# Kernel optimization log

Measured on AMD Instinct MI355X. Metric: run time of the kernel, lower is better.

The kernel has to match this reference:

```python
import jax, jax.numpy as jnp
import numpy as np

N, M, D, G, E = 1024, 1024, 1024, 16, 64  # rois, ref rois, feat_dim, groups, emb_dim
DG = D // G  # 64 per-group dim


def _make_boxes(k, n):
    k1, k2 = jax.random.split(k)
    xy = jax.random.uniform(k1, (n, 2), dtype=jnp.float32) * 500.0
    wh = jax.random.uniform(k2, (n, 2), dtype=jnp.float32) * 100.0 + 1.0
    return jnp.concatenate([xy, xy + wh], axis=1)  # [n,4] xmin,ymin,xmax,ymax


def setup_inputs() -> dict:
    key = jax.random.key(0)
    ks = jax.random.split(key, 10)
    s = 0.02
    return {
        "roi_feat": jax.random.normal(ks[0], (N, D), dtype=jnp.float32),
        "ref_feat": jax.random.normal(ks[1], (M, D), dtype=jnp.float32),
        "rois1": _make_boxes(ks[2], N),
        "rois2": _make_boxes(ks[3], M),
        "Wq": jax.random.normal(ks[4], (D, D), dtype=jnp.float32) * s,
        "bq": jnp.zeros((D,), jnp.float32),
        "Wk": jax.random.normal(ks[5], (D, D), dtype=jnp.float32) * s,
        "bk": jnp.zeros((D,), jnp.float32),
        "Wg": jax.random.normal(ks[6], (G, E), dtype=jnp.float32) * s,
        "bg": jnp.zeros((G,), jnp.float32),
        "Wv": jax.random.normal(ks[7], (G, DG, D), dtype=jnp.float32) * s,
        "bv": jnp.zeros((D,), jnp.float32),
    }


def _position_matrix(bbox, ref_bbox):
    # bbox [N,4], ref_bbox [M,4] -> [N,M,4]
    def parts(b):
        xmin, ymin, xmax, ymax = b[:, 0], b[:, 1], b[:, 2], b[:, 3]
        w = xmax - xmin + 1.0
        h = ymax - ymin + 1.0
        cx = 0.5 * (xmin + xmax)
        cy = 0.5 * (ymin + ymax)
        return w, h, cx, cy

    w, h, cx, cy = parts(bbox)            # [N]
    wr, hr, cxr, cyr = parts(ref_bbox)    # [M]
    dx = jnp.log(jnp.abs((cx[:, None] - cxr[None, :]) / w[:, None]) + 1e-3)
    dy = jnp.log(jnp.abs((cy[:, None] - cyr[None, :]) / h[:, None]) + 1e-3)
    dw = jnp.log(w[:, None] / wr[None, :])
    dh = jnp.log(h[:, None] / hr[None, :])
    return jnp.stack([dx, dy, dw, dh], axis=2)  # [N,M,4]


def _position_embedding(pos_mat, feat_dim=64, wave_length=1000.0):
    fr = jnp.arange(feat_dim // 8, dtype=jnp.float32)            # [8]
    dim_mat = jnp.power(wave_length, (8.0 / feat_dim) * fr)      # [8]
    div = pos_mat[..., None] * 100.0 / dim_mat                   # [N,M,4,8]
    emb = jnp.concatenate([jnp.sin(div), jnp.cos(div)], axis=3)  # [N,M,4,16]
    return emb.reshape(pos_mat.shape[0], pos_mat.shape[1], -1)   # [N,M,64]


def reference(roi_feat, ref_feat, rois1, rois2, Wq, bq, Wk, bk, Wg, bg, Wv, bv):
    # position embedding: [N,M,E]
    pos_emb = _position_embedding(_position_matrix(rois1, rois2), feat_dim=E)
    # Wgs 1x1 conv (E -> G) + relu -> aff_weight [N,G,M]
    aff_weight = jax.nn.relu(jnp.einsum("nme,ge->ngm", pos_emb, Wg) + bg[None, :, None])
    # grouped q/k projections
    q = (roi_feat @ Wq + bq).reshape(N, G, DG)   # [N,G,dg]
    k = (ref_feat @ Wk + bk).reshape(M, G, DG)   # [M,G,dg]
    aff = jnp.einsum("ngd,mgd->ngm", q, k) * (1.0 / np.sqrt(DG))
    weighted = jnp.log(aff_weight + 1e-6) + aff  # [N,G,M]
    sm = jax.nn.softmax(weighted, axis=2)
    out_t = jnp.einsum("ngm,md->ngd", sm, ref_feat)          # [N,G,D]
    out = jnp.einsum("ngd,god->ngo", out_t, Wv).reshape(N, D) + bv  # grouped 1x1 conv
    return out
```

## Files before the change

kernel.cpp:

```cpp
#include <hip/hip_runtime.h>
#include <hip/hip_fp16.h>
#include <cstddef>

#define N_ 1024
#define M_ 1024
#define D_ 1024
#define G_ 16
#define DG_ 64

typedef __bf16 bf16x8 __attribute__((ext_vector_type(8)));
typedef _Float16 f16x8 __attribute__((ext_vector_type(8)));
typedef float f32x4 __attribute__((ext_vector_type(4)));

__device__ __forceinline__ size_t qkf_idx(int g, int rb, int ks, int lane) {
    return ((((size_t)(g * 64 + rb)) * 2 + ks) * 64 + lane) * 8;
}
__device__ __forceinline__ size_t vf_idx(int g, int ot, int mc, int lane) {
    return ((((size_t)(g * 4 + ot)) * 32 + mc) * 64 + lane) * 8;
}
__device__ __forceinline__ size_t awt_idx(int g, int mb, int n, int quad) {
    return (((size_t)(g * 64 + mb)) * 1024 + n) * 16 + quad * 4;
}

__global__ __launch_bounds__(256)
void transpose_cast(const float* __restrict__ Wq, const float* __restrict__ Wk,
                    __bf16* __restrict__ WqT, __bf16* __restrict__ WkT)
{
    __shared__ float t[64][65];
    const float* src = blockIdx.z ? Wk : Wq;
    __bf16* dst = blockIdx.z ? WkT : WqT;
    const int i0 = blockIdx.x * 64, j0 = blockIdx.y * 64;
    const int tid = threadIdx.x;
    const int r = tid >> 4, c4 = (tid & 15) * 4;
    #pragma unroll
    for (int it = 0; it < 4; ++it) {
        float4 a = *(const float4*)&src[(size_t)(i0 + r + it * 16) * D_ + j0 + c4];
        t[r + it * 16][c4 + 0] = a.x; t[r + it * 16][c4 + 1] = a.y;
        t[r + it * 16][c4 + 2] = a.z; t[r + it * 16][c4 + 3] = a.w;
    }
    __syncthreads();
    #pragma unroll
    for (int it = 0; it < 4; ++it) {
        const int row = r + it * 16;
        __bf16 p[4];
        #pragma unroll
        for (int q = 0; q < 4; ++q) p[q] = (__bf16)t[c4 + q][row];
        *(uint2*)&dst[(size_t)(j0 + row) * D_ + i0 + c4] = *(const uint2*)p;
    }
}

__global__ __launch_bounds__(256)
void cast_wv(const float* __restrict__ Wv, __bf16* __restrict__ out)
{
    const int idx = blockIdx.x * 256 + threadIdx.x;
    float4 a = *(const float4*)&Wv[(size_t)idx * 4];
    __bf16 p[4] = {(__bf16)a.x, (__bf16)a.y, (__bf16)a.z, (__bf16)a.w};
    *(uint2*)&out[(size_t)idx * 4] = *(const uint2*)p;
}

__global__ __launch_bounds__(256)
void gemm_mfma(const float* __restrict__ roi, const float* __restrict__ ref,
               const __bf16* __restrict__ WqT, const __bf16* __restrict__ WkT,
               const __bf16* __restrict__ Wvb,
               const float* __restrict__ bq, const float* __restrict__ bk,
               __bf16* __restrict__ Qf, __bf16* __restrict__ Kf,
               __bf16* __restrict__ Vf)
{
    __shared__ __bf16 As[128][72];
    __shared__ __bf16 Bs[128][72];
    const int z = blockIdx.z;
    const float* A = (z == 0) ? roi : ref;
    const __bf16* B = (z == 0) ? WqT : (z == 1) ? WkT : Wvb;
    const int tid = threadIdx.x;
    const int i0 = blockIdx.x * 128, j0 = blockIdx.y * 128;
    const int w = tid >> 6, lane = tid & 63;
    const int quad = lane >> 4, l15 = lane & 15;
    const int iw = (w & 1) * 64, jw = (w >> 1) * 64;

    f32x4 acc[4][4] = {};

    for (int k0 = 0; k0 < D_; k0 += 64) {
        __syncthreads();
        #pragma unroll
        for (int it = 0; it < 8; ++it) {
            const int idx = tid + 256 * it;
            const int row = idx >> 4, c = idx & 15;
            float4 a = *(const float4*)&A[(size_t)(i0 + row) * D_ + k0 + c * 4];
            __bf16* d = &As[row][c * 4];
            d[0] = (__bf16)a.x; d[1] = (__bf16)a.y; d[2] = (__bf16)a.z; d[3] = (__bf16)a.w;
        }
        #pragma unroll
        for (int it = 0; it < 4; ++it) {
            const int idx = tid + 256 * it;
            const int row = idx >> 3, c = idx & 7;
            *(uint4*)&Bs[row][c * 8] = *(const uint4*)&B[(size_t)(j0 + row) * D_ + k0 + c * 8];
        }
        __syncthreads();
        #pragma unroll
        for (int ks = 0; ks < 2; ++ks) {
            bf16x8 af[4], bfr[4];
            #pragma unroll
            for (int t = 0; t < 4; ++t) {
                af[t]  = *(const bf16x8*)&As[iw + t * 16 + l15][ks * 32 + quad * 8];
                bfr[t] = *(const bf16x8*)&Bs[jw + t * 16 + l15][ks * 32 + quad * 8];
            }
            #pragma unroll
            for (int ti = 0; ti < 4; ++ti)
                #pragma unroll
                for (int tj = 0; tj < 4; ++tj)
                    acc[ti][tj] = __builtin_amdgcn_mfma_f32_16x16x32_bf16(
                        af[ti], bfr[tj], acc[ti][tj], 0, 0, 0);
        }
    }

    if (z < 2) {
        const float* bias = (z == 0) ? bq : bk;
        __bf16* dst = (z == 0) ? Qf : Kf;
        const float scale = (z == 0) ? 0.125f : 1.0f;
        #pragma unroll
        for (int ti = 0; ti < 4; ++ti) {
            const int rbase = i0 + iw + ti * 16;
            const int rb = rbase >> 4;
            #pragma unroll
            for (int tj = 0; tj < 4; ++tj) {
                const int go = j0 + jw + tj * 16 + l15;
                const int g = go >> 6, ks = (go >> 5) & 1;
                const int lanef = ((go >> 3) & 3) * 16;
                const int jf = go & 7;
                const float bb = bias[go];
                __bf16* base = dst + qkf_idx(g, rb, ks, 0) + jf;
                #pragma unroll
                for (int r = 0; r < 4; ++r)
                    base[(size_t)(lanef + quad * 4 + r) * 8] =
                        (__bf16)((acc[ti][tj][r] + bb) * scale);
            }
        }
    } else {
        #pragma unroll
        for (int ti = 0; ti < 4; ++ti) {
            const int mbase = i0 + iw + ti * 16 + quad * 4;
            const int mc = mbase >> 5, quadv = (mbase >> 3) & 3, jb = mbase & 7;
            #pragma unroll
            for (int tj = 0; tj < 4; ++tj) {
                const int go = j0 + jw + tj * 16 + l15;
                const int g = go >> 6, ot = (go >> 4) & 3, o15 = go & 15;
                __bf16 p[4];
                #pragma unroll
                for (int r = 0; r < 4; ++r) p[r] = (__bf16)acc[ti][tj][r];
                *(uint2*)&Vf[vf_idx(g, ot, mc, quadv * 16 + o15) + jb] = *(const uint2*)p;
            }
        }
    }
}

__global__ __launch_bounds__(256)
void posbias_mfma(const float* __restrict__ rois1, const float* __restrict__ rois2,
                  const float* __restrict__ Wg, const float* __restrict__ bg,
                  __half* __restrict__ AWt)
{
    const int tid = threadIdx.x;
    const int w = tid >> 6, lane = tid & 63;
    const int quad = lane >> 4, l15 = lane & 15;
    const int n = blockIdx.y;
    const int m0w = blockIdx.x * 256 + w * 64;

    const float xmin = rois1[n * 4 + 0], ymin = rois1[n * 4 + 1];
    const float xmax = rois1[n * 4 + 2], ymax = rois1[n * 4 + 3];
    const float wn  = xmax - xmin + 1.f, hn  = ymax - ymin + 1.f;
    const float cxn = 0.5f * (xmin + xmax), cyn = 0.5f * (ymin + ymax);

    f16x8 wgf[2];
    #pragma unroll
    for (int ks = 0; ks < 2; ++ks) {
        const float* p = &Wg[l15 * 64 + ks * 32 + quad * 8];
        float4 a = *(const float4*)p;
        float4 b = *(const float4*)(p + 4);
        wgf[ks][0] = (_Float16)a.x; wgf[ks][1] = (_Float16)a.y;
        wgf[ks][2] = (_Float16)a.z; wgf[ks][3] = (_Float16)a.w;
        wgf[ks][4] = (_Float16)b.x; wgf[ks][5] = (_Float16)b.y;
        wgf[ks][6] = (_Float16)b.z; wgf[ks][7] = (_Float16)b.w;
    }
    const float bgv = bg[l15];

    const float fr8[8] = {100.0f, 42.16965f, 17.782794f, 7.4989421f,
                          3.1622777f, 1.3335214f, 0.56234133f, 0.23713737f};
    const float phase = (quad & 1) ? 1.5707963267948966f : 0.f;

    #pragma unroll
    for (int ti = 0; ti < 4; ++ti) {
        const int mt0 = m0w + ti * 16;
        const int m = mt0 + l15;
        float4 r2 = *(const float4*)&rois2[m * 4];
        const float wr  = r2.z - r2.x + 1.f, hr  = r2.w - r2.y + 1.f;
        const float cxr = 0.5f * (r2.x + r2.z), cyr = 0.5f * (r2.y + r2.w);

        const float f0 = __logf(fabsf((cxn - cxr) / wn) + 0.001f);
        const float f1 = __logf(fabsf((cyn - cyr) / hn) + 0.001f);
        const float f2 = __logf(wn / wr);
        const float f3 = __logf(hn / hr);
        const float fa = (quad & 2) ? f1 : f0;
        const float fb = (quad & 2) ? f3 : f2;

        f32x4 acc = {};
        #pragma unroll
        for (int ks = 0; ks < 2; ++ks) {
            const float feat = ks ? fb : fa;
            f16x8 ef;
            #pragma unroll
            for (int j = 0; j < 8; ++j)
                ef[j] = (_Float16)__sinf(fmaf(feat, fr8[j], phase));
            acc = __builtin_amdgcn_mfma_f32_16x16x32_f16(ef, wgf[ks], acc, 0, 0, 0);
        }

        __half p[4];
        #pragma unroll
        for (int r = 0; r < 4; ++r)
            p[r] = __float2half(fmaxf(acc[r] + bgv, 0.f) + 1e-6f);
        *(uint2*)&AWt[awt_idx(l15, mt0 >> 4, n, quad)] = *(const uint2*)p;
    }
}

__global__ __launch_bounds__(256)
void attn_mfma(const __bf16* __restrict__ Qf, const __bf16* __restrict__ Kf,
               const __bf16* __restrict__ Vf, const __half* __restrict__ AWt,
               const float* __restrict__ bv, float* __restrict__ out)
{
    __shared__ __bf16 Ps[4][2][16][72];
    __shared__ float accb[4][64][17];
    __shared__ float lsb[4][16];

    const int tid = threadIdx.x;
    const int w = tid >> 6, lane = tid & 63;
    const int quad = lane >> 4, l15 = lane & 15;
    const int nb = blockIdx.x, n0 = nb * 16, g = blockIdx.y;

    bf16x8 qf[2];
    qf[0] = *(const bf16x8*)&Qf[qkf_idx(g, nb, 0, lane)];
    qf[1] = *(const bf16x8*)&Qf[qkf_idx(g, nb, 1, lane)];

    f32x4 acc[4] = {};
    float llocal = 0.f;

    #pragma unroll
    for (int t64 = 0; t64 < 4; ++t64) {
        const int mt = w * 4 + t64;
        const int buf = t64 & 1;

        f32x4 s[4];
        #pragma unroll
        for (int t = 0; t < 4; ++t) {
            bf16x8 ka0 = *(const bf16x8*)&Kf[qkf_idx(g, mt * 4 + t, 0, lane)];
            bf16x8 ka1 = *(const bf16x8*)&Kf[qkf_idx(g, mt * 4 + t, 1, lane)];
            f32x4 z = {};
            z = __builtin_amdgcn_mfma_f32_16x16x32_bf16(ka0, qf[0], z, 0, 0, 0);
            s[t] = __builtin_amdgcn_mfma_f32_16x16x32_bf16(ka1, qf[1], z, 0, 0, 0);
        }

        #pragma unroll
        for (int t = 0; t < 4; ++t) {
            uint2 au = *(const uint2*)&AWt[awt_idx(g, mt * 4 + t, n0 + l15, quad)];
            const __half* a4 = (const __half*)&au;
            __bf16 pk[4];
            #pragma unroll
            for (int r = 0; r < 4; ++r) {
                const float p = __half2float(a4[r]) * __expf(s[t][r]);
                llocal += p;
                pk[r] = (__bf16)p;
            }
            *(uint2*)&Ps[w][buf][l15][t * 16 + quad * 4] = *(const uint2*)pk;
        }

        #pragma unroll
        for (int mcl = 0; mcl < 2; ++mcl) {
            bf16x8 pb = *(const bf16x8*)&Ps[w][buf][l15][mcl * 32 + quad * 8];
            #pragma unroll
            for (int ot = 0; ot < 4; ++ot) {
                bf16x8 va = *(const bf16x8*)&Vf[vf_idx(g, ot, mt * 2 + mcl, lane)];
                acc[ot] = __builtin_amdgcn_mfma_f32_16x16x32_bf16(va, pb, acc[ot], 0, 0, 0);
            }
        }
    }

    llocal += __shfl_xor(llocal, 16, 64);
    llocal += __shfl_xor(llocal, 32, 64);

    #pragma unroll
    for (int ot = 0; ot < 4; ++ot)
        #pragma unroll
        for (int r = 0; r < 4; ++r)
            accb[w][ot * 16 + quad * 4 + r][l15] = acc[ot][r];
    if (quad == 0) lsb[w][l15] = llocal;
    __syncthreads();

    const float lt = lsb[0][l15] + lsb[1][l15] + lsb[2][l15] + lsb[3][l15];
    const float inv = 1.f / lt;
    #pragma unroll
    for (int r = 0; r < 4; ++r) {
        const int o = w * 16 + quad * 4 + r;
        const int ogl = g * 64 + o;
        const float v = accb[0][o][l15] + accb[1][o][l15] +
                        accb[2][o][l15] + accb[3][o][l15];
        out[(size_t)(n0 + l15) * D_ + ogl] = v * inv + bv[ogl];
    }
}

extern "C" void kernel_launch(void* const* d_in, const int* in_sizes, int n_in,
                              void* d_out, int out_size, void* d_ws, size_t ws_size,
                              hipStream_t stream) {
    const float* roi_feat = (const float*)d_in[0];
    const float* ref_feat = (const float*)d_in[1];
    const float* rois1    = (const float*)d_in[2];
    const float* rois2    = (const float*)d_in[3];
    const float* Wq       = (const float*)d_in[4];
    const float* bq       = (const float*)d_in[5];
    const float* Wk       = (const float*)d_in[6];
    const float* bk       = (const float*)d_in[7];
    const float* Wg       = (const float*)d_in[8];
    const float* bg       = (const float*)d_in[9];
    const float* Wv       = (const float*)d_in[10];
    const float* bv       = (const float*)d_in[11];
    float* out = (float*)d_out;

    char* ws = (char*)d_ws;
    __bf16* WqT = (__bf16*)(ws + 0);
    __bf16* WkT = (__bf16*)(ws + (2u << 20));
    __bf16* Wvb = (__bf16*)(ws + (4u << 20));
    __bf16* Qf  = (__bf16*)(ws + (6u << 20));
    __bf16* Kf  = (__bf16*)(ws + (8u << 20));
    __bf16* Vf  = (__bf16*)(ws + (10u << 20));
    __half* AWt = (__half*)(ws + (12u << 20));

    dim3 blk(256);
    transpose_cast<<<dim3(16, 16, 2), blk, 0, stream>>>(Wq, Wk, WqT, WkT);
    cast_wv<<<dim3(1024), blk, 0, stream>>>(Wv, Wvb);
    posbias_mfma<<<dim3(4, 1024), blk, 0, stream>>>(rois1, rois2, Wg, bg, AWt);
    gemm_mfma<<<dim3(8, 8, 3), blk, 0, stream>>>(roi_feat, ref_feat, WqT, WkT, Wvb,
                                                 bq, bk, Qf, Kf, Vf);
    attn_mfma<<<dim3(64, 16), blk, 0, stream>>>(Qf, Kf, Vf, AWt, bv, out);
}
```

Before: 163.0 us.

## Double-buffer GEMM tiles, stage outputs through LDS, use row-major intermediates

```diff
diff --git a/kernel.cpp b/kernel.cpp
--- a/kernel.cpp
+++ b/kernel.cpp
@@ -12,26 +12,31 @@
 typedef _Float16 f16x8 __attribute__((ext_vector_type(8)));
 typedef float f32x4 __attribute__((ext_vector_type(4)));
 
-__device__ __forceinline__ size_t qkf_idx(int g, int rb, int ks, int lane) {
-    return ((((size_t)(g * 64 + rb)) * 2 + ks) * 64 + lane) * 8;
-}
-__device__ __forceinline__ size_t vf_idx(int g, int ot, int mc, int lane) {
-    return ((((size_t)(g * 4 + ot)) * 32 + mc) * 64 + lane) * 8;
-}
-__device__ __forceinline__ size_t awt_idx(int g, int mb, int n, int quad) {
-    return (((size_t)(g * 64 + mb)) * 1024 + n) * 16 + quad * 4;
-}
-
 __global__ __launch_bounds__(256)
-void transpose_cast(const float* __restrict__ Wq, const float* __restrict__ Wk,
-                    __bf16* __restrict__ WqT, __bf16* __restrict__ WkT)
+void prep_weights(const float* __restrict__ Wq, const float* __restrict__ Wk,
+                  const float* __restrict__ Wv,
+                  __bf16* __restrict__ WqT, __bf16* __restrict__ WkT,
+                  __bf16* __restrict__ Wvb)
 {
-    __shared__ float t[64][65];
-    const float* src = blockIdx.z ? Wk : Wq;
-    __bf16* dst = blockIdx.z ? WkT : WqT;
+    const int z = blockIdx.z;
     const int i0 = blockIdx.x * 64, j0 = blockIdx.y * 64;
     const int tid = threadIdx.x;
     const int r = tid >> 4, c4 = (tid & 15) * 4;
+
+    if (z == 2) {
+        #pragma unroll
+        for (int it = 0; it < 4; ++it) {
+            const int row = r + it * 16;
+            float4 a = *(const float4*)&Wv[(size_t)(i0 + row) * D_ + j0 + c4];
+            __bf16 p[4] = {(__bf16)a.x, (__bf16)a.y, (__bf16)a.z, (__bf16)a.w};
+            *(uint2*)&Wvb[(size_t)(i0 + row) * D_ + j0 + c4] = *(const uint2*)p;
+        }
+        return;
+    }
+
+    __shared__ float t[64][65];
+    const float* src = z ? Wk : Wq;
+    __bf16* dst = z ? WkT : WqT;
     #pragma unroll
     for (int it = 0; it < 4; ++it) {
         float4 a = *(const float4*)&src[(size_t)(i0 + r + it * 16) * D_ + j0 + c4];
@@ -49,25 +54,19 @@
     }
 }
 
-__global__ __launch_bounds__(256)
-void cast_wv(const float* __restrict__ Wv, __bf16* __restrict__ out)
-{
-    const int idx = blockIdx.x * 256 + threadIdx.x;
-    float4 a = *(const float4*)&Wv[(size_t)idx * 4];
-    __bf16 p[4] = {(__bf16)a.x, (__bf16)a.y, (__bf16)a.z, (__bf16)a.w};
-    *(uint2*)&out[(size_t)idx * 4] = *(const uint2*)p;
-}
-
-__global__ __launch_bounds__(256)
+#define GP 72
+#define CTP 136
+
+__global__ __launch_bounds__(256, 1)
 void gemm_mfma(const float* __restrict__ roi, const float* __restrict__ ref,
                const __bf16* __restrict__ WqT, const __bf16* __restrict__ WkT,
                const __bf16* __restrict__ Wvb,
                const float* __restrict__ bq, const float* __restrict__ bk,
-               __bf16* __restrict__ Qf, __bf16* __restrict__ Kf,
-               __bf16* __restrict__ Vf)
+               __bf16* __restrict__ qout, __bf16* __restrict__ kout,
+               __bf16* __restrict__ Vt)
 {
-    __shared__ __bf16 As[128][72];
-    __shared__ __bf16 Bs[128][72];
+    __shared__ __align__(16) char smem[2 * 2 * 128 * GP * 2];
+
     const int z = blockIdx.z;
     const float* A = (z == 0) ? roi : ref;
     const __bf16* B = (z == 0) ? WqT : (z == 1) ? WkT : Wvb;
@@ -77,32 +76,56 @@
     const int quad = lane >> 4, l15 = lane & 15;
     const int iw = (w & 1) * 64, jw = (w >> 1) * 64;
 
+    const int arow = tid >> 4, ac = (tid & 15) * 4;
+    const int brow = tid >> 3, bc = (tid & 7) * 8;
+
     f32x4 acc[4][4] = {};
-
-    for (int k0 = 0; k0 < D_; k0 += 64) {
-        __syncthreads();
+    float4 ra[8];
+    uint4 rb[4];
+
+    auto As = [&](int buf) { return (__bf16(*)[GP])(smem + buf * 36864); };
+    auto Bs = [&](int buf) { return (__bf16(*)[GP])(smem + buf * 36864 + 18432); };
+
+    auto load_tile = [&](int kt) {
+        const int k0 = kt * 64;
+        #pragma unroll
+        for (int it = 0; it < 8; ++it)
+            ra[it] = *(const float4*)&A[(size_t)(i0 + arow + it * 16) * D_ + k0 + ac];
+        #pragma unroll
+        for (int it = 0; it < 4; ++it)
+            rb[it] = *(const uint4*)&B[(size_t)(j0 + brow + it * 32) * D_ + k0 + bc];
+    };
+    auto write_tile = [&](int buf) {
+        __bf16(*as)[GP] = As(buf);
+        __bf16(*bs)[GP] = Bs(buf);
         #pragma unroll
         for (int it = 0; it < 8; ++it) {
-            const int idx = tid + 256 * it;
-            const int row = idx >> 4, c = idx & 15;
-            float4 a = *(const float4*)&A[(size_t)(i0 + row) * D_ + k0 + c * 4];
-            __bf16* d = &As[row][c * 4];
-            d[0] = (__bf16)a.x; d[1] = (__bf16)a.y; d[2] = (__bf16)a.z; d[3] = (__bf16)a.w;
-        }
-        #pragma unroll
-        for (int it = 0; it < 4; ++it) {
-            const int idx = tid + 256 * it;
-            const int row = idx >> 3, c = idx & 7;
-            *(uint4*)&Bs[row][c * 8] = *(const uint4*)&B[(size_t)(j0 + row) * D_ + k0 + c * 8];
-        }
-        __syncthreads();
+            __bf16 p[4] = {(__bf16)ra[it].x, (__bf16)ra[it].y,
+                           (__bf16)ra[it].z, (__bf16)ra[it].w};
+            *(uint2*)&as[arow + it * 16][ac] = *(const uint2*)p;
+        }
+        #pragma unroll
+        for (int it = 0; it < 4; ++it)
+            *(uint4*)&bs[brow + it * 32][bc] = rb[it];
+    };
+
+    load_tile(0);
+    write_tile(0);
+    __syncthreads();
+
+    for (int kt = 0; kt < 16; ++kt) {
+        const int buf = kt & 1;
+        if (kt < 15) load_tile(kt + 1);
+
+        __bf16(*as)[GP] = As(buf);
+        __bf16(*bs)[GP] = Bs(buf);
         #pragma unroll
         for (int ks = 0; ks < 2; ++ks) {
             bf16x8 af[4], bfr[4];
             #pragma unroll
             for (int t = 0; t < 4; ++t) {
-                af[t]  = *(const bf16x8*)&As[iw + t * 16 + l15][ks * 32 + quad * 8];
-                bfr[t] = *(const bf16x8*)&Bs[jw + t * 16 + l15][ks * 32 + quad * 8];
+                af[t]  = *(const bf16x8*)&as[iw + t * 16 + l15][ks * 32 + quad * 8];
+                bfr[t] = *(const bf16x8*)&bs[jw + t * 16 + l15][ks * 32 + quad * 8];
             }
             #pragma unroll
             for (int ti = 0; ti < 4; ++ti)
@@ -111,53 +134,58 @@
                     acc[ti][tj] = __builtin_amdgcn_mfma_f32_16x16x32_bf16(
                         af[ti], bfr[tj], acc[ti][tj], 0, 0, 0);
         }
-    }
+
+        if (kt < 15) write_tile(buf ^ 1);
+        __syncthreads();
+    }
+
+    __bf16(*Ct)[CTP] = (__bf16(*)[CTP])smem;
 
     if (z < 2) {
         const float* bias = (z == 0) ? bq : bk;
-        __bf16* dst = (z == 0) ? Qf : Kf;
         const float scale = (z == 0) ? 0.125f : 1.0f;
         #pragma unroll
-        for (int ti = 0; ti < 4; ++ti) {
-            const int rbase = i0 + iw + ti * 16;
-            const int rb = rbase >> 4;
+        for (int ti = 0; ti < 4; ++ti)
             #pragma unroll
             for (int tj = 0; tj < 4; ++tj) {
-                const int go = j0 + jw + tj * 16 + l15;
-                const int g = go >> 6, ks = (go >> 5) & 1;
-                const int lanef = ((go >> 3) & 3) * 16;
-                const int jf = go & 7;
-                const float bb = bias[go];
-                __bf16* base = dst + qkf_idx(g, rb, ks, 0) + jf;
+                const int col = jw + tj * 16 + l15;
+                const float bb = bias[j0 + col];
                 #pragma unroll
                 for (int r = 0; r < 4; ++r)
-                    base[(size_t)(lanef + quad * 4 + r) * 8] =
+                    Ct[iw + ti * 16 + quad * 4 + r][col] =
                         (__bf16)((acc[ti][tj][r] + bb) * scale);
             }
-        }
     } else {
         #pragma unroll
-        for (int ti = 0; ti < 4; ++ti) {
-            const int mbase = i0 + iw + ti * 16 + quad * 4;
-            const int mc = mbase >> 5, quadv = (mbase >> 3) & 3, jb = mbase & 7;
+        for (int ti = 0; ti < 4; ++ti)
             #pragma unroll
             for (int tj = 0; tj < 4; ++tj) {
-                const int go = j0 + jw + tj * 16 + l15;
-                const int g = go >> 6, ot = (go >> 4) & 3, o15 = go & 15;
+                const int col = jw + tj * 16 + l15;
+                const int row0 = iw + ti * 16 + quad * 4;
                 __bf16 p[4];
                 #pragma unroll
                 for (int r = 0; r < 4; ++r) p[r] = (__bf16)acc[ti][tj][r];
-                *(uint2*)&Vf[vf_idx(g, ot, mc, quadv * 16 + o15) + jb] = *(const uint2*)p;
-            }
-        }
-    }
+                *(uint2*)&Ct[col][row0] = *(const uint2*)p;
+            }
+    }
+    __syncthreads();
+
+    __bf16* dst = (z == 0) ? qout : (z == 1) ? kout : Vt;
+    const int orow = tid >> 1, ohalf = (tid & 1) * 64;
+    __bf16* gp = dst + (size_t)((z < 2 ? i0 : j0) + orow) * 1024 +
+                 (z < 2 ? j0 : i0) + ohalf;
+    #pragma unroll
+    for (int c = 0; c < 8; ++c)
+        *(uint4*)&gp[c * 8] = *(const uint4*)&Ct[orow][ohalf + c * 8];
 }
 
 __global__ __launch_bounds__(256)
 void posbias_mfma(const float* __restrict__ rois1, const float* __restrict__ rois2,
                   const float* __restrict__ Wg, const float* __restrict__ bg,
-                  __half* __restrict__ AWt)
+                  __half* __restrict__ aw)
 {
+    __shared__ __half pt[4][16][72];
+
     const int tid = threadIdx.x;
     const int w = tid >> 6, lane = tid & 63;
     const int quad = lane >> 4, l15 = lane & 15;
@@ -216,13 +244,18 @@
         #pragma unroll
         for (int r = 0; r < 4; ++r)
             p[r] = __float2half(fmaxf(acc[r] + bgv, 0.f) + 1e-6f);
-        *(uint2*)&AWt[awt_idx(l15, mt0 >> 4, n, quad)] = *(const uint2*)p;
-    }
+        *(uint2*)&pt[w][l15][ti * 16 + quad * 4] = *(const uint2*)p;
+    }
+
+    const int gg = lane >> 2, mseg = (lane & 3) * 16;
+    __half* dst = aw + (size_t)gg * N_ * M_ + (size_t)n * M_ + m0w + mseg;
+    *(uint4*)&dst[0] = *(const uint4*)&pt[w][gg][mseg];
+    *(uint4*)&dst[8] = *(const uint4*)&pt[w][gg][mseg + 8];
 }
 
 __global__ __launch_bounds__(256)
-void attn_mfma(const __bf16* __restrict__ Qf, const __bf16* __restrict__ Kf,
-               const __bf16* __restrict__ Vf, const __half* __restrict__ AWt,
+void attn_mfma(const __bf16* __restrict__ qb, const __bf16* __restrict__ kb,
+               const __bf16* __restrict__ Vt, const __half* __restrict__ aw,
                const float* __restrict__ bv, float* __restrict__ out)
 {
     __shared__ __bf16 Ps[4][2][16][72];
@@ -235,8 +268,8 @@
     const int nb = blockIdx.x, n0 = nb * 16, g = blockIdx.y;
 
     bf16x8 qf[2];
-    qf[0] = *(const bf16x8*)&Qf[qkf_idx(g, nb, 0, lane)];
-    qf[1] = *(const bf16x8*)&Qf[qkf_idx(g, nb, 1, lane)];
+    qf[0] = *(const bf16x8*)&qb[(size_t)(n0 + l15) * D_ + g * 64 + quad * 8];
+    qf[1] = *(const bf16x8*)&qb[(size_t)(n0 + l15) * D_ + g * 64 + 32 + quad * 8];
 
     f32x4 acc[4] = {};
     float llocal = 0.f;
@@ -244,21 +277,24 @@
     #pragma unroll
     for (int t64 = 0; t64 < 4; ++t64) {
         const int mt = w * 4 + t64;
+        const int m0 = mt * 64;
         const int buf = t64 & 1;
 
         f32x4 s[4];
         #pragma unroll
         for (int t = 0; t < 4; ++t) {
-            bf16x8 ka0 = *(const bf16x8*)&Kf[qkf_idx(g, mt * 4 + t, 0, lane)];
-            bf16x8 ka1 = *(const bf16x8*)&Kf[qkf_idx(g, mt * 4 + t, 1, lane)];
-            f32x4 z = {};
-            z = __builtin_amdgcn_mfma_f32_16x16x32_bf16(ka0, qf[0], z, 0, 0, 0);
-            s[t] = __builtin_amdgcn_mfma_f32_16x16x32_bf16(ka1, qf[1], z, 0, 0, 0);
+            const __bf16* kr = &kb[(size_t)(m0 + t * 16 + l15) * D_ + g * 64 + quad * 8];
+            bf16x8 ka0 = *(const bf16x8*)kr;
+            bf16x8 ka1 = *(const bf16x8*)(kr + 32);
+            f32x4 zz = {};
+            zz = __builtin_amdgcn_mfma_f32_16x16x32_bf16(ka0, qf[0], zz, 0, 0, 0);
+            s[t] = __builtin_amdgcn_mfma_f32_16x16x32_bf16(ka1, qf[1], zz, 0, 0, 0);
         }
 
         #pragma unroll
         for (int t = 0; t < 4; ++t) {
-            uint2 au = *(const uint2*)&AWt[awt_idx(g, mt * 4 + t, n0 + l15, quad)];
+            uint2 au = *(const uint2*)&aw[((size_t)g * N_ + n0 + l15) * M_ +
+                                          m0 + t * 16 + quad * 4];
             const __half* a4 = (const __half*)&au;
             __bf16 pk[4];
             #pragma unroll
@@ -275,7 +311,8 @@
             bf16x8 pb = *(const bf16x8*)&Ps[w][buf][l15][mcl * 32 + quad * 8];
             #pragma unroll
             for (int ot = 0; ot < 4; ++ot) {
-                bf16x8 va = *(const bf16x8*)&Vf[vf_idx(g, ot, mt * 2 + mcl, lane)];
+                bf16x8 va = *(const bf16x8*)&Vt[(size_t)(g * 64 + ot * 16 + l15) * M_ +
+                                                m0 + mcl * 32 + quad * 8];
                 acc[ot] = __builtin_amdgcn_mfma_f32_16x16x32_bf16(va, pb, acc[ot], 0, 0, 0);
             }
         }
@@ -322,19 +359,18 @@
     float* out = (float*)d_out;
 
     char* ws = (char*)d_ws;
-    __bf16* WqT = (__bf16*)(ws + 0);
-    __bf16* WkT = (__bf16*)(ws + (2u << 20));
-    __bf16* Wvb = (__bf16*)(ws + (4u << 20));
-    __bf16* Qf  = (__bf16*)(ws + (6u << 20));
-    __bf16* Kf  = (__bf16*)(ws + (8u << 20));
-    __bf16* Vf  = (__bf16*)(ws + (10u << 20));
-    __half* AWt = (__half*)(ws + (12u << 20));
+    __bf16* WqT  = (__bf16*)(ws + 0);
+    __bf16* WkT  = (__bf16*)(ws + (2u << 20));
+    __bf16* Wvb  = (__bf16*)(ws + (4u << 20));
+    __bf16* qbuf = (__bf16*)(ws + (6u << 20));
+    __bf16* kbuf = (__bf16*)(ws + (8u << 20));
+    __bf16* Vtb  = (__bf16*)(ws + (10u << 20));
+    __half* aw   = (__half*)(ws + (12u << 20));
 
     dim3 blk(256);
-    transpose_cast<<<dim3(16, 16, 2), blk, 0, stream>>>(Wq, Wk, WqT, WkT);
-    cast_wv<<<dim3(1024), blk, 0, stream>>>(Wv, Wvb);
-    posbias_mfma<<<dim3(4, 1024), blk, 0, stream>>>(rois1, rois2, Wg, bg, AWt);
+    prep_weights<<<dim3(16, 16, 3), blk, 0, stream>>>(Wq, Wk, Wv, WqT, WkT, Wvb);
+    posbias_mfma<<<dim3(4, 1024), blk, 0, stream>>>(rois1, rois2, Wg, bg, aw);
     gemm_mfma<<<dim3(8, 8, 3), blk, 0, stream>>>(roi_feat, ref_feat, WqT, WkT, Wvb,
-                                                 bq, bk, Qf, Kf, Vf);
-    attn_mfma<<<dim3(64, 16), blk, 0, stream>>>(Qf, Kf, Vf, AWt, bv, out);
-}
+                                                 bq, bk, qbuf, kbuf, Vtb);
+    attn_mfma<<<dim3(64, 16), blk, 0, stream>>>(qbuf, kbuf, Vtb, aw, bv, out);
+}
```

Measured after the change: 191.2 us. 1.17x slower.

## Merge weight-prep kernels and run GEMM and posbias in one launch

Applied to the files above, without the earlier changes.

```diff
diff --git a/kernel.cpp b/kernel.cpp
--- a/kernel.cpp
+++ b/kernel.cpp
@@ -23,15 +23,30 @@
 }
 
 __global__ __launch_bounds__(256)
-void transpose_cast(const float* __restrict__ Wq, const float* __restrict__ Wk,
-                    __bf16* __restrict__ WqT, __bf16* __restrict__ WkT)
+void prep_weights(const float* __restrict__ Wq, const float* __restrict__ Wk,
+                  const float* __restrict__ Wv,
+                  __bf16* __restrict__ WqT, __bf16* __restrict__ WkT,
+                  __bf16* __restrict__ Wvb)
 {
-    __shared__ float t[64][65];
-    const float* src = blockIdx.z ? Wk : Wq;
-    __bf16* dst = blockIdx.z ? WkT : WqT;
+    const int z = blockIdx.z;
     const int i0 = blockIdx.x * 64, j0 = blockIdx.y * 64;
     const int tid = threadIdx.x;
     const int r = tid >> 4, c4 = (tid & 15) * 4;
+
+    if (z == 2) {
+        #pragma unroll
+        for (int it = 0; it < 4; ++it) {
+            const int row = r + it * 16;
+            float4 a = *(const float4*)&Wv[(size_t)(i0 + row) * D_ + j0 + c4];
+            __bf16 p[4] = {(__bf16)a.x, (__bf16)a.y, (__bf16)a.z, (__bf16)a.w};
+            *(uint2*)&Wvb[(size_t)(i0 + row) * D_ + j0 + c4] = *(const uint2*)p;
+        }
+        return;
+    }
+
+    __shared__ float t[64][65];
+    const float* src = z ? Wk : Wq;
+    __bf16* dst = z ? WkT : WqT;
     #pragma unroll
     for (int it = 0; it < 4; ++it) {
         float4 a = *(const float4*)&src[(size_t)(i0 + r + it * 16) * D_ + j0 + c4];
@@ -50,119 +65,114 @@
 }
 
 __global__ __launch_bounds__(256)
-void cast_wv(const float* __restrict__ Wv, __bf16* __restrict__ out)
-{
-    const int idx = blockIdx.x * 256 + threadIdx.x;
-    float4 a = *(const float4*)&Wv[(size_t)idx * 4];
-    __bf16 p[4] = {(__bf16)a.x, (__bf16)a.y, (__bf16)a.z, (__bf16)a.w};
-    *(uint2*)&out[(size_t)idx * 4] = *(const uint2*)p;
-}
-
-__global__ __launch_bounds__(256)
-void gemm_mfma(const float* __restrict__ roi, const float* __restrict__ ref,
+void fused_mid(const float* __restrict__ roi, const float* __restrict__ ref,
                const __bf16* __restrict__ WqT, const __bf16* __restrict__ WkT,
                const __bf16* __restrict__ Wvb,
                const float* __restrict__ bq, const float* __restrict__ bk,
                __bf16* __restrict__ Qf, __bf16* __restrict__ Kf,
-               __bf16* __restrict__ Vf)
+               __bf16* __restrict__ Vf,
+               const float* __restrict__ rois1, const float* __restrict__ rois2,
+               const float* __restrict__ Wg, const float* __restrict__ bg,
+               __half* __restrict__ AWt)
 {
-    __shared__ __bf16 As[128][72];
-    __shared__ __bf16 Bs[128][72];
-    const int z = blockIdx.z;
-    const float* A = (z == 0) ? roi : ref;
-    const __bf16* B = (z == 0) ? WqT : (z == 1) ? WkT : Wvb;
-    const int tid = threadIdx.x;
-    const int i0 = blockIdx.x * 128, j0 = blockIdx.y * 128;
-    const int w = tid >> 6, lane = tid & 63;
-    const int quad = lane >> 4, l15 = lane & 15;
-    const int iw = (w & 1) * 64, jw = (w >> 1) * 64;
-
-    f32x4 acc[4][4] = {};
-
-    for (int k0 = 0; k0 < D_; k0 += 64) {
-        __syncthreads();
-        #pragma unroll
-        for (int it = 0; it < 8; ++it) {
-            const int idx = tid + 256 * it;
-            const int row = idx >> 4, c = idx & 15;
-            float4 a = *(const float4*)&A[(size_t)(i0 + row) * D_ + k0 + c * 4];
-            __bf16* d = &As[row][c * 4];
-            d[0] = (__bf16)a.x; d[1] = (__bf16)a.y; d[2] = (__bf16)a.z; d[3] = (__bf16)a.w;
-        }
-        #pragma unroll
-        for (int it = 0; it < 4; ++it) {
-            const int idx = tid + 256 * it;
-            const int row = idx >> 3, c = idx & 7;
-            *(uint4*)&Bs[row][c * 8] = *(const uint4*)&B[(size_t)(j0 + row) * D_ + k0 + c * 8];
-        }
-        __syncthreads();
-        #pragma unroll
-        for (int ks = 0; ks < 2; ++ks) {
-            bf16x8 af[4], bfr[4];
-            #pragma unroll
-            for (int t = 0; t < 4; ++t) {
-                af[t]  = *(const bf16x8*)&As[iw + t * 16 + l15][ks * 32 + quad * 8];
-                bfr[t] = *(const bf16x8*)&Bs[jw + t * 16 + l15][ks * 32 + quad * 8];
-            }
-            #pragma unroll
-            for (int ti = 0; ti < 4; ++ti)
-                #pragma unroll
-                for (int tj = 0; tj < 4; ++tj)
-                    acc[ti][tj] = __builtin_amdgcn_mfma_f32_16x16x32_bf16(
-                        af[ti], bfr[tj], acc[ti][tj], 0, 0, 0);
-        }
-    }
-
-    if (z < 2) {
-        const float* bias = (z == 0) ? bq : bk;
-        __bf16* dst = (z == 0) ? Qf : Kf;
-        const float scale = (z == 0) ? 0.125f : 1.0f;
-        #pragma unroll
-        for (int ti = 0; ti < 4; ++ti) {
-            const int rbase = i0 + iw + ti * 16;
-            const int rb = rbase >> 4;
-            #pragma unroll
-            for (int tj = 0; tj < 4; ++tj) {
-                const int go = j0 + jw + tj * 16 + l15;
-                const int g = go >> 6, ks = (go >> 5) & 1;
-                const int lanef = ((go >> 3) & 3) * 16;
-                const int jf = go & 7;
-                const float bb = bias[go];
-                __bf16* base = dst + qkf_idx(g, rb, ks, 0) + jf;
-                #pragma unroll
-                for (int r = 0; r < 4; ++r)
-                    base[(size_t)(lanef + quad * 4 + r) * 8] =
-                        (__bf16)((acc[ti][tj][r] + bb) * scale);
-            }
-        }
-    } else {
-        #pragma unroll
-        for (int ti = 0; ti < 4; ++ti) {
-            const int mbase = i0 + iw + ti * 16 + quad * 4;
-            const int mc = mbase >> 5, quadv = (mbase >> 3) & 3, jb = mbase & 7;
-            #pragma unroll
-            for (int tj = 0; tj < 4; ++tj) {
-                const int go = j0 + jw + tj * 16 + l15;
-                const int g = go >> 6, ot = (go >> 4) & 3, o15 = go & 15;
-                __bf16 p[4];
-                #pragma unroll
-                for (int r = 0; r < 4; ++r) p[r] = (__bf16)acc[ti][tj][r];
-                *(uint2*)&Vf[vf_idx(g, ot, mc, quadv * 16 + o15) + jb] = *(const uint2*)p;
-            }
-        }
-    }
-}
-
-__global__ __launch_bounds__(256)
-void posbias_mfma(const float* __restrict__ rois1, const float* __restrict__ rois2,
-                  const float* __restrict__ Wg, const float* __restrict__ bg,
-                  __half* __restrict__ AWt)
-{
+    __shared__ __align__(16) char smem[36864];
+    const int b = blockIdx.x;
     const int tid = threadIdx.x;
     const int w = tid >> 6, lane = tid & 63;
     const int quad = lane >> 4, l15 = lane & 15;
-    const int n = blockIdx.y;
-    const int m0w = blockIdx.x * 256 + w * 64;
+
+    if (b < 192) {
+        const int z = b >> 6, t6 = b & 63;
+        const float* A = (z == 0) ? roi : ref;
+        const __bf16* B = (z == 0) ? WqT : (z == 1) ? WkT : Wvb;
+        const int i0 = (t6 >> 3) * 128, j0 = (t6 & 7) * 128;
+        const int iw = (w & 1) * 64, jw = (w >> 1) * 64;
+
+        __bf16(*As)[72] = (__bf16(*)[72])smem;
+        __bf16(*Bs)[72] = (__bf16(*)[72])(smem + 18432);
+
+        f32x4 acc[4][4] = {};
+
+        for (int k0 = 0; k0 < D_; k0 += 64) {
+            __syncthreads();
+            #pragma unroll
+            for (int it = 0; it < 8; ++it) {
+                const int idx = tid + 256 * it;
+                const int row = idx >> 4, c = idx & 15;
+                float4 a = *(const float4*)&A[(size_t)(i0 + row) * D_ + k0 + c * 4];
+                __bf16* d = &As[row][c * 4];
+                d[0] = (__bf16)a.x; d[1] = (__bf16)a.y;
+                d[2] = (__bf16)a.z; d[3] = (__bf16)a.w;
+            }
+            #pragma unroll
+            for (int it = 0; it < 4; ++it) {
+                const int idx = tid + 256 * it;
+                const int row = idx >> 3, c = idx & 7;
+                *(uint4*)&Bs[row][c * 8] =
+                    *(const uint4*)&B[(size_t)(j0 + row) * D_ + k0 + c * 8];
+            }
+            __syncthreads();
+            #pragma unroll
+            for (int ks = 0; ks < 2; ++ks) {
+                bf16x8 af[4], bfr[4];
+                #pragma unroll
+                for (int t = 0; t < 4; ++t) {
+                    af[t]  = *(const bf16x8*)&As[iw + t * 16 + l15][ks * 32 + quad * 8];
+                    bfr[t] = *(const bf16x8*)&Bs[jw + t * 16 + l15][ks * 32 + quad * 8];
+                }
+                #pragma unroll
+                for (int ti = 0; ti < 4; ++ti)
+                    #pragma unroll
+                    for (int tj = 0; tj < 4; ++tj)
+                        acc[ti][tj] = __builtin_amdgcn_mfma_f32_16x16x32_bf16(
+                            af[ti], bfr[tj], acc[ti][tj], 0, 0, 0);
+            }
+        }
+
+        if (z < 2) {
+            const float* bias = (z == 0) ? bq : bk;
+            __bf16* dst = (z == 0) ? Qf : Kf;
+            const float scale = (z == 0) ? 0.125f : 1.0f;
+            #pragma unroll
+            for (int ti = 0; ti < 4; ++ti) {
+                const int rb = (i0 + iw + ti * 16) >> 4;
+                #pragma unroll
+                for (int tj = 0; tj < 4; ++tj) {
+                    const int go = j0 + jw + tj * 16 + l15;
+                    const int g = go >> 6, ks = (go >> 5) & 1;
+                    const int lanef = ((go >> 3) & 3) * 16;
+                    const int jf = go & 7;
+                    const float bb = bias[go];
+                    __bf16* base = dst + qkf_idx(g, rb, ks, 0) + jf;
+                    #pragma unroll
+                    for (int r = 0; r < 4; ++r)
+                        base[(size_t)(lanef + quad * 4 + r) * 8] =
+                            (__bf16)((acc[ti][tj][r] + bb) * scale);
+                }
+            }
+        } else {
+            #pragma unroll
+            for (int ti = 0; ti < 4; ++ti) {
+                const int mbase = i0 + iw + ti * 16 + quad * 4;
+                const int mc = mbase >> 5, quadv = (mbase >> 3) & 3, jb = mbase & 7;
+                #pragma unroll
+                for (int tj = 0; tj < 4; ++tj) {
+                    const int go = j0 + jw + tj * 16 + l15;
+                    const int g = go >> 6, ot = (go >> 4) & 3, o15 = go & 15;
+                    __bf16 p[4];
+                    #pragma unroll
+                    for (int r = 0; r < 4; ++r) p[r] = (__bf16)acc[ti][tj][r];
+                    *(uint2*)&Vf[vf_idx(g, ot, mc, quadv * 16 + o15) + jb] =
+                        *(const uint2*)p;
+                }
+            }
+        }
+        return;
+    }
+
+    const int pb = b - 192;
+    const int n = pb >> 2;
+    const int m0w = (pb & 3) * 256 + w * 64;
 
     const float xmin = rois1[n * 4 + 0], ymin = rois1[n * 4 + 1];
     const float xmax = rois1[n * 4 + 2], ymax = rois1[n * 4 + 3];
@@ -174,11 +184,11 @@
     for (int ks = 0; ks < 2; ++ks) {
         const float* p = &Wg[l15 * 64 + ks * 32 + quad * 8];
         float4 a = *(const float4*)p;
-        float4 b = *(const float4*)(p + 4);
+        float4 bb = *(const float4*)(p + 4);
         wgf[ks][0] = (_Float16)a.x; wgf[ks][1] = (_Float16)a.y;
         wgf[ks][2] = (_Float16)a.z; wgf[ks][3] = (_Float16)a.w;
-        wgf[ks][4] = (_Float16)b.x; wgf[ks][5] = (_Float16)b.y;
-        wgf[ks][6] = (_Float16)b.z; wgf[ks][7] = (_Float16)b.w;
+        wgf[ks][4] = (_Float16)bb.x; wgf[ks][5] = (_Float16)bb.y;
+        wgf[ks][6] = (_Float16)bb.z; wgf[ks][7] = (_Float16)bb.w;
     }
     const float bgv = bg[l15];
 
@@ -272,11 +282,11 @@
 
         #pragma unroll
         for (int mcl = 0; mcl < 2; ++mcl) {
-            bf16x8 pb = *(const bf16x8*)&Ps[w][buf][l15][mcl * 32 + quad * 8];
+            bf16x8 pbf = *(const bf16x8*)&Ps[w][buf][l15][mcl * 32 + quad * 8];
             #pragma unroll
             for (int ot = 0; ot < 4; ++ot) {
                 bf16x8 va = *(const bf16x8*)&Vf[vf_idx(g, ot, mt * 2 + mcl, lane)];
-                acc[ot] = __builtin_amdgcn_mfma_f32_16x16x32_bf16(va, pb, acc[ot], 0, 0, 0);
+                acc[ot] = __builtin_amdgcn_mfma_f32_16x16x32_bf16(va, pbf, acc[ot], 0, 0, 0);
             }
         }
     }
@@ -331,10 +341,9 @@
     __half* AWt = (__half*)(ws + (12u << 20));
 
     dim3 blk(256);
-    transpose_cast<<<dim3(16, 16, 2), blk, 0, stream>>>(Wq, Wk, WqT, WkT);
-    cast_wv<<<dim3(1024), blk, 0, stream>>>(Wv, Wvb);
-    posbias_mfma<<<dim3(4, 1024), blk, 0, stream>>>(rois1, rois2, Wg, bg, AWt);
-    gemm_mfma<<<dim3(8, 8, 3), blk, 0, stream>>>(roi_feat, ref_feat, WqT, WkT, Wvb,
-                                                 bq, bk, Qf, Kf, Vf);
+    prep_weights<<<dim3(16, 16, 3), blk, 0, stream>>>(Wq, Wk, Wv, WqT, WkT, Wvb);
+    fused_mid<<<dim3(4288), blk, 0, stream>>>(roi_feat, ref_feat, WqT, WkT, Wvb,
+                                              bq, bk, Qf, Kf, Vf,
+                                              rois1, rois2, Wg, bg, AWt);
     attn_mfma<<<dim3(64, 16), blk, 0, stream>>>(Qf, Kf, Vf, AWt, bv, out);
 }
```

Measured after the change: 153.5 us. -5.8%, faster.
